# Performance work log

Measured on AMD Instinct MI355X. Metric: run time of the kernel, lower is better.

## Reference

```python
import jax, jax.numpy as jnp
import numpy as np

MARGIN = 1.0


def setup_inputs() -> dict:
    key = jax.random.key(0)
    k1, k2 = jax.random.split(key)
    scores = jax.random.normal(k1, (512, 512), dtype=jnp.float32)
    labels = jax.random.randint(k2, (512, 512), 0, 2, dtype=jnp.int64)
    return {"scores": scores, "labels": labels}


def reference(scores, labels):
    # pos/neg masks per batch row
    pos = labels == 1  # (B, N)
    neg = labels == 0  # (B, N)
    # pairwise diff: pos score minus neg score -> (B, N_pos_axis, N_neg_axis)
    diff = scores[:, :, None] - scores[:, None, :]
    pair_mask = pos[:, :, None] & neg[:, None, :]
    hinge = jnp.maximum(MARGIN - diff, 0.0)
    total = jnp.sum(jnp.where(pair_mask, hinge, 0.0))
    num_pairs = jnp.sum(pair_mask)
    return jnp.where(num_pairs > 0, total / num_pairs, 0.0)
```

## Files before the change

### kernel.cpp

```cpp
#include <hip/hip_runtime.h>

#define ROWN 512
constexpr float MARGIN = 1.0f;

__global__ __launch_bounds__(256) void pmrl_rows(const float* __restrict__ scores,
                                                 const int* __restrict__ labels,
                                                 float* __restrict__ row_sum,
                                                 unsigned int* __restrict__ row_pairs) {
    __shared__ float pos_s[ROWN];
    __shared__ float neg_s[ROWN];
    __shared__ int cnts[2];
    __shared__ float wsum[4];

    const int row = blockIdx.x;
    const int t   = threadIdx.x;

    if (t < 2) cnts[t] = 0;
    __syncthreads();

    const float* s = scores + (size_t)row * ROWN;
    const int*   l = labels + (size_t)row * ROWN;

    for (int i = t; i < ROWN; i += 256) {
        float v   = s[i];
        int   lab = l[i];
        if (lab == 1) {
            int idx = atomicAdd(&cnts[0], 1);
            pos_s[idx] = v;
        } else if (lab == 0) {
            int idx = atomicAdd(&cnts[1], 1);
            neg_s[idx] = v;
        }
    }
    __syncthreads();

    const int P = cnts[0];
    const int Q = cnts[1];

    float acc = 0.0f;
    for (int i = t; i < P; i += 256) {
        const float base = MARGIN - pos_s[i];
        float local = 0.0f;
        for (int j = 0; j < Q; ++j) {
            local += fmaxf(base + neg_s[j], 0.0f);
        }
        acc += local;
    }

    #pragma unroll
    for (int off = 32; off > 0; off >>= 1) acc += __shfl_down(acc, off, 64);
    if ((t & 63) == 0) wsum[t >> 6] = acc;
    __syncthreads();

    if (t == 0) {
        row_sum[row]   = wsum[0] + wsum[1] + wsum[2] + wsum[3];
        row_pairs[row] = (unsigned int)(P * Q);
    }
}

__global__ __launch_bounds__(64) void pmrl_final(const float* __restrict__ row_sum,
                                                 const unsigned int* __restrict__ row_pairs,
                                                 float* __restrict__ out) {
    const int t = threadIdx.x;
    double s = 0.0;
    unsigned long long pc = 0ull;
    for (int i = t; i < ROWN; i += 64) {
        s  += (double)row_sum[i];
        pc += (unsigned long long)row_pairs[i];
    }
    #pragma unroll
    for (int off = 32; off > 0; off >>= 1) {
        s  += __shfl_down(s, off, 64);
        pc += __shfl_down(pc, off, 64);
    }
    if (t == 0) {
        out[0] = (pc > 0ull) ? (float)(s / (double)pc) : 0.0f;
    }
}

extern "C" void kernel_launch(void* const* d_in, const int* in_sizes, int n_in,
                              void* d_out, int out_size, void* d_ws, size_t ws_size,
                              hipStream_t stream) {
    const float* scores = (const float*)d_in[0];
    const int*   labels = (const int*)d_in[1];
    float*       out    = (float*)d_out;

    float*        row_sum   = (float*)d_ws;
    unsigned int* row_pairs = (unsigned int*)((char*)d_ws + ROWN * sizeof(float));

    pmrl_rows<<<ROWN, 256, 0, stream>>>(scores, labels, row_sum, row_pairs);
    pmrl_final<<<1, 64, 0, stream>>>(row_sum, row_pairs, out);
}
```

Before: 65.72 us.

## Use wave-ballot compaction and float4 vectorized inner loop with padding

Replaces the per-element shared-memory atomic compaction with a wave-level ballot/popcount scheme that issues one atomic per wave per class. The inner pairwise loop now reads negatives as float4 from LDS into four independent accumulators, with the negative array padded with a large negative sentinel so that padded slots contribute zero. This is meant to cut LDS atomic contention, LDS load count and the serial add dependency chain in the hot loop, at the cost of an extra barrier and a changed summation order.

```diff
diff --git a/kernel.cpp b/kernel.cpp
--- a/kernel.cpp
+++ b/kernel.cpp
@@ -2,18 +2,20 @@
 
 #define ROWN 512
 constexpr float MARGIN = 1.0f;
+constexpr float NEG_INF = -1e30f;
 
 __global__ __launch_bounds__(256) void pmrl_rows(const float* __restrict__ scores,
                                                  const int* __restrict__ labels,
                                                  float* __restrict__ row_sum,
                                                  unsigned int* __restrict__ row_pairs) {
     __shared__ float pos_s[ROWN];
-    __shared__ float neg_s[ROWN];
+    __shared__ float neg_s[ROWN + 4];
     __shared__ int cnts[2];
     __shared__ float wsum[4];
 
-    const int row = blockIdx.x;
-    const int t   = threadIdx.x;
+    const int row  = blockIdx.x;
+    const int t    = threadIdx.x;
+    const int lane = t & 63;
 
     if (t < 2) cnts[t] = 0;
     __syncthreads();
@@ -21,39 +23,60 @@
     const float* s = scores + (size_t)row * ROWN;
     const int*   l = labels + (size_t)row * ROWN;
 
-    for (int i = t; i < ROWN; i += 256) {
-        float v   = s[i];
-        int   lab = l[i];
-        if (lab == 1) {
-            int idx = atomicAdd(&cnts[0], 1);
-            pos_s[idx] = v;
-        } else if (lab == 0) {
-            int idx = atomicAdd(&cnts[1], 1);
-            neg_s[idx] = v;
+    #pragma unroll
+    for (int r = 0; r < 2; ++r) {
+        const int i   = t + r * 256;
+        const float v = s[i];
+        const int lab = l[i];
+        const bool isp = (lab == 1);
+        const bool isn = (lab == 0);
+        const unsigned long long bp = __ballot(isp);
+        const unsigned long long bn = __ballot(isn);
+        const unsigned long long ltmask = (1ull << lane) - 1ull;
+        const int pp = __popcll(bp & ltmask);
+        const int pn = __popcll(bn & ltmask);
+        int basep = 0, basen = 0;
+        if (lane == 0) {
+            basep = atomicAdd(&cnts[0], __popcll(bp));
+            basen = atomicAdd(&cnts[1], __popcll(bn));
         }
+        basep = __shfl(basep, 0, 64);
+        basen = __shfl(basen, 0, 64);
+        if (isp) pos_s[basep + pp] = v;
+        if (isn) neg_s[basen + pn] = v;
     }
     __syncthreads();
 
     const int P = cnts[0];
     const int Q = cnts[1];
 
+    const int pad = (4 - (Q & 3)) & 3;
+    if (t < pad) neg_s[Q + t] = NEG_INF;
+    __syncthreads();
+    const int Q4 = (Q + 3) >> 2;
+
     float acc = 0.0f;
+    const float4* neg4 = (const float4*)neg_s;
     for (int i = t; i < P; i += 256) {
-        const float base = MARGIN - pos_s[i];
-        float local = 0.0f;
-        for (int j = 0; j < Q; ++j) {
-            local += fmaxf(base + neg_s[j], 0.0f);
+        const float c = MARGIN - pos_s[i];
+        float a0 = 0.f, a1 = 0.f, a2 = 0.f, a3 = 0.f;
+        for (int j = 0; j < Q4; ++j) {
+            const float4 n = neg4[j];
+            a0 += fmaxf(c + n.x, 0.0f);
+            a1 += fmaxf(c + n.y, 0.0f);
+            a2 += fmaxf(c + n.z, 0.0f);
+            a3 += fmaxf(c + n.w, 0.0f);
         }
-        acc += local;
+        acc += (a0 + a1) + (a2 + a3);
     }
 
     #pragma unroll
     for (int off = 32; off > 0; off >>= 1) acc += __shfl_down(acc, off, 64);
-    if ((t & 63) == 0) wsum[t >> 6] = acc;
+    if (lane == 0) wsum[t >> 6] = acc;
     __syncthreads();
 
     if (t == 0) {
-        row_sum[row]   = wsum[0] + wsum[1] + wsum[2] + wsum[3];
+        row_sum[row]   = (wsum[0] + wsum[1]) + (wsum[2] + wsum[3]);
         row_pairs[row] = (unsigned int)(P * Q);
     }
 }
```

Result: faster. 64.22 us (-2.3%).
